# Kernel tuning notes

Hardware: AMD Instinct MI355X
Metric: run time of the kernel (lower is better)

Reference implementation:

```python
import jax, jax.numpy as jnp
import numpy as np

BATCH, SEQ, DIM, DSTATE = 8, 2048, 1024, 16


def setup_inputs() -> dict:
    key = jax.random.key(0)
    ks = jax.random.split(key, 8)
    u = jax.random.normal(ks[0], (BATCH, SEQ, DIM), jnp.float32)
    gate = jax.random.normal(ks[1], (BATCH, SEQ, DIM), jnp.float32)
    # parameters (init per module: normal std=0.01 for A_log/B/C, zeros for D)
    A_log = 0.01 * jax.random.normal(ks[2], (DSTATE, DSTATE), jnp.float32)
    B_mat = 0.01 * jax.random.normal(ks[3], (DIM, DSTATE), jnp.float32)
    C_mat = 0.01 * jax.random.normal(ks[4], (DIM, DSTATE), jnp.float32)
    D = jnp.zeros((DIM,), jnp.float32)
    bound = 1.0 / np.sqrt(DIM)  # nn.Linear default init
    dt_w = jax.random.uniform(ks[5], (1, DIM), jnp.float32, -bound, bound)
    dt_b = jax.random.uniform(ks[6], (1,), jnp.float32, -bound, bound)
    return {"u": u, "gate": gate, "A_log": A_log, "B_mat": B_mat,
            "C_mat": C_mat, "D": D, "dt_w": dt_w, "dt_b": dt_b}


def reference(u, gate, A_log, B_mat, C_mat, D, dt_w, dt_b):
    # delta = sigmoid(Linear(gate)) : [B, S, 1] -> [B, S]
    delta = jax.nn.sigmoid(jnp.einsum('bsd,od->bso', gate, dt_w) + dt_b)[..., 0]
    A = -jnp.exp(A_log)                               # [N, N]
    scaled_A = delta[..., None, None] * A             # [B, S, N, N]
    A_exp = jax.scipy.linalg.expm(scaled_A)           # batched matrix exp
    Bu = jnp.einsum('bsd,dn->bsn', u, B_mat)          # [B, S, N]

    def step(h, inp):
        Aexp_t, bu_t = inp                            # [B,N,N], [B,N]
        h = jnp.einsum('bn,bnm->bm', h, Aexp_t) + bu_t
        return h, h

    h0 = jnp.zeros((u.shape[0], DSTATE), u.dtype)
    _, hs = jax.lax.scan(step, h0, (jnp.swapaxes(A_exp, 0, 1), jnp.swapaxes(Bu, 0, 1)))
    hs = jnp.swapaxes(hs, 0, 1)                       # [B, S, N]
    y = jnp.einsum('bsn,dn->bsd', hs, C_mat) + D * u  # [B, S, D]
    return y
```

## Files before the change

### kernel.cpp

```cpp
#include <hip/hip_runtime.h>

#define BATCH  8
#define SEQ    2048
#define DIMSZ  1024
#define NST    16
#define LCH    32
#define CPB    (SEQ / LCH)
#define NCHUNK (BATCH * CPB)
#define NCHEB  32
#define PI_F   3.14159265358979f

typedef __attribute__((ext_vector_type(8))) short bf16x8;
typedef __attribute__((ext_vector_type(4))) float f32x4;

static __device__ __forceinline__ unsigned short f2bf(float f) {
    unsigned u = __builtin_bit_cast(unsigned, f);
    unsigned r = (u + 0x7FFFu + ((u >> 16) & 1u)) >> 16;
    return (unsigned short)r;
}
static __device__ __forceinline__ float bf2f(unsigned short h) {
    unsigned u = ((unsigned)h) << 16;
    return __builtin_bit_cast(float, u);
}

__global__ __launch_bounds__(256) void sA_nodes(
    const float* __restrict__ A_log, float* __restrict__ Fn)
{
    __shared__ float Xs[16 * 17];
    __shared__ float Ts[16 * 17];
    const int tid = threadIdx.x;
    const int i = tid >> 4, j = tid & 15;
    const float th = (2.f * blockIdx.x + 1.f) * (PI_F / 64.f);
    const float dl = 0.5f * (1.f + cosf(th));
    const float a  = -expf(A_log[tid]);
    const float x  = dl * a * (1.0f / 64.0f);
    Xs[i*17 + j] = x;
    Ts[i*17 + j] = x;
    float S = x + (i == j ? 1.0f : 0.0f);
    __syncthreads();
#pragma unroll
    for (int k = 2; k <= 8; ++k) {
        float nt = 0.f;
#pragma unroll
        for (int kk = 0; kk < 16; ++kk)
            nt = fmaf(Ts[i*17 + kk], Xs[kk*17 + j], nt);
        nt *= (1.0f / (float)k);
        S += nt;
        __syncthreads();
        Ts[i*17 + j] = nt;
        __syncthreads();
    }
#pragma unroll
    for (int r = 0; r < 6; ++r) {
        __syncthreads();
        Ts[i*17 + j] = S;
        __syncthreads();
        float nt = 0.f;
#pragma unroll
        for (int kk = 0; kk < 16; ++kk)
            nt = fmaf(Ts[i*17 + kk], Ts[kk*17 + j], nt);
        S = nt;
    }
    Fn[(size_t)blockIdx.x * 256 + tid] = S;
}

__global__ __launch_bounds__(256) void sB_setup(
    const float* __restrict__ Fn, const float* __restrict__ B_mat,
    float* __restrict__ Gt,
    unsigned short* __restrict__ Bfh, unsigned short* __restrict__ Bfl)
{
    const int tid = threadIdx.x;
    const int blk = blockIdx.x;
    if (blk < NCHEB) {
        const int m = blk;
        float acc = 0.f;
        for (int k = 0; k < NCHEB; ++k) {
            const float th = (2.f * k + 1.f) * (PI_F / 64.f);
            acc = fmaf(Fn[(size_t)k * 256 + tid], cosf(m * th), acc);
        }
        const float sc = (m == 0) ? (1.f / 32.f) : (2.f / 32.f);
        Gt[(size_t)tid * NCHEB + m] = acc * sc;
    } else {
        const int idx0 = (blk - NCHEB) * 2048;
        for (int t = 0; t < 8; ++t) {
            const int idx = idx0 + t * 256 + tid;
            const int j  = idx & 7;
            const int l  = (idx >> 3) & 63;
            const int ks = idx >> 9;
            const int k  = ks * 32 + ((l >> 4) << 3) + j;
            const int n  = l & 15;
            float bv = B_mat[(size_t)k * 16 + n];
            unsigned short h = f2bf(bv);
            Bfh[idx] = h;
            Bfl[idx] = f2bf(bv - bf2f(h));
        }
    }
}

__global__ __launch_bounds__(256) void k1a_delta(
    const float* __restrict__ gate, const float* __restrict__ dt_w,
    const float* __restrict__ dt_b, float* __restrict__ delta)
{
    const int tid  = threadIdx.x;
    const int lane = tid & 63;
    const int w    = tid >> 6;
    const int tok  = blockIdx.x * 4 + w;
    const float* gp = gate + (size_t)tok * DIMSZ;
    float s = 0.f;
#pragma unroll
    for (int i = 0; i < 4; ++i) {
        const float4 g  = *(const float4*)(gp   + i * 256 + lane * 4);
        const float4 wv = *(const float4*)(dt_w + i * 256 + lane * 4);
        s = fmaf(g.x, wv.x, s); s = fmaf(g.y, wv.y, s);
        s = fmaf(g.z, wv.z, s); s = fmaf(g.w, wv.w, s);
    }
#pragma unroll
    for (int off = 32; off >= 1; off >>= 1)
        s += __shfl_xor(s, off, 64);
    if (lane == 0)
        delta[tok] = 1.0f / (1.0f + expf(-(s + dt_b[0])));
}

__global__ __launch_bounds__(512, 2) void kBA3(
    const float* __restrict__ u,
    const unsigned short* __restrict__ Bfh, const unsigned short* __restrict__ Bfl,
    const float* __restrict__ Gt, const float* __restrict__ delta,
    float* __restrict__ Bu, float* __restrict__ P, float* __restrict__ e)
{
    __shared__ float smem[8704];
    __shared__ float Bus[LCH * NST];
    __shared__ float dl[LCH];
    __shared__ float sd[1];
    __shared__ float Ps[16 * 17];
    const int tid  = threadIdx.x;
    const int lane = tid & 63;
    const int w    = tid >> 6;
    const size_t gI = blockIdx.x;
    const int tok0 = (int)gI * 32;
    const int qk   = w & 3;
    const int tt   = w >> 2;
    const int q    = lane >> 4;
    const int r    = lane & 15;

    if (tid < LCH) dl[tid] = delta[gI * LCH + tid];

    const uint4* bh = (const uint4*)Bfh;
    const uint4* bl = (const uint4*)Bfl;

    const float* up = u + (size_t)(tok0 + tt * 16 + r) * DIMSZ + qk * 256 + q * 8;

    f32x4 acc = {0.f, 0.f, 0.f, 0.f};
#pragma unroll
    for (int c = 0; c < 8; ++c) {
        const float4 v0 = *(const float4*)(up + c * 32);
        const float4 v1 = *(const float4*)(up + c * 32 + 4);
        const uint4 FH = bh[(qk * 8 + c) * 64 + lane];
        const uint4 FL = bl[(qk * 8 + c) * 64 + lane];
        const float fu[8] = {v0.x, v0.y, v0.z, v0.w, v1.x, v1.y, v1.z, v1.w};
        bf16x8 uh, ul;
#pragma unroll
        for (int i = 0; i < 8; ++i) {
            unsigned short h = f2bf(fu[i]);
            uh[i] = (short)h;
            ul[i] = (short)f2bf(fu[i] - bf2f(h));
        }
        const bf16x8 Bh = __builtin_bit_cast(bf16x8, FH);
        const bf16x8 Bl = __builtin_bit_cast(bf16x8, FL);
        acc = __builtin_amdgcn_mfma_f32_16x16x32_bf16(uh, Bh, acc, 0, 0, 0);
        acc = __builtin_amdgcn_mfma_f32_16x16x32_bf16(uh, Bl, acc, 0, 0, 0);
        acc = __builtin_amdgcn_mfma_f32_16x16x32_bf16(ul, Bh, acc, 0, 0, 0);
    }

    float* red = smem;
#pragma unroll
    for (int rr = 0; rr < 4; ++rr)
        red[w * 256 + (q * 4 + rr) * 16 + r] = acc[rr];
    __syncthreads();
    const int rb = (tid >> 8) * 1024 + (tid & 255);
    const float bv = red[rb] + red[rb + 256] + red[rb + 512] + red[rb + 768];
    Bu[gI * 512 + tid] = bv;
    Bus[tid] = bv;

    const int el = tid & 255;
    float gr[NCHEB];
    {
        const float4* gp = (const float4*)(Gt + (size_t)el * NCHEB);
#pragma unroll
        for (int qq = 0; qq < NCHEB / 4; ++qq) {
            float4 v = gp[qq];
            gr[qq*4+0] = v.x; gr[qq*4+1] = v.y; gr[qq*4+2] = v.z; gr[qq*4+3] = v.w;
        }
    }
    __syncthreads();
    if (tid == 0) {
        float s = 0.f;
        for (int t = 0; t < LCH; ++t) s += dl[t];
        sd[0] = s;
    }
    const int tgrp = tid >> 8;
    for (int t = tgrp * 16; t < tgrp * 16 + 16; ++t) {
        const float x = 2.f * dl[t] - 1.f;
        float accm = fmaf(gr[1], x, gr[0]);
        float tm2 = 1.f, tm1 = x;
#pragma unroll
        for (int m = 2; m < NCHEB; ++m) {
            const float tm = fmaf(2.f * x, tm1, -tm2);
            accm = fmaf(gr[m], tm, accm);
            tm2 = tm1; tm1 = tm;
        }
        smem[t * 272 + (el >> 4) * 17 + (el & 15)] = accm;
    }
    __syncthreads();
    float S;
    {
        const float xp = 2.f * (sd[0] * (1.f / LCH)) - 1.f;
        float accm = fmaf(gr[1], xp, gr[0]);
        float tm2 = 1.f, tm1 = xp;
#pragma unroll
        for (int m = 2; m < NCHEB; ++m) {
            const float tm = fmaf(2.f * xp, tm1, -tm2);
            accm = fmaf(gr[m], tm, accm);
            tm2 = tm1; tm1 = tm;
        }
        S = accm;
    }
    const int i = el >> 4, j = el & 15;
#pragma unroll
    for (int rr = 0; rr < 5; ++rr) {
        if (tid < 256) Ps[i*17 + j] = S;
        __syncthreads();
        float ns = 0.f;
#pragma unroll
        for (int k = 0; k < 16; ++k)
            ns = fmaf(Ps[i*17 + k], Ps[k*17 + j], ns);
        __syncthreads();
        S = ns;
    }
    if (tid < 256) P[gI * 256 + tid] = S;
    if (tid < 64) {
        const int gq = tid >> 4, jj = tid & 15, i0 = gq * 4;
        float h = 0.f;
        for (int t = 0; t < LCH; ++t) {
            float pp = 0.f;
#pragma unroll
            for (int m = 0; m < 4; ++m)
                pp = fmaf(__shfl(h, gq * 20 + m, 64),
                          smem[t * 272 + (i0 + m) * 17 + jj], pp);
            pp += __shfl_xor(pp, 16, 64);
            pp += __shfl_xor(pp, 32, 64);
            h = Bus[t * 16 + jj] + pp;
        }
        if (gq == 0) e[gI * NST + jj] = h;
    }
}

__global__ __launch_bounds__(256) void k4_scan(
    const float* __restrict__ P, const float* __restrict__ e,
    float* __restrict__ hin)
{
    __shared__ float Pl[32 * 272];
    __shared__ float el[32 * NST];
    const int tid = threadIdx.x;
    const int b = blockIdx.x;
    float h = 0.f;
    for (int half = 0; half < 2; ++half) {
        const int c0 = half * 32;
        for (int idx = tid; idx < 32*256; idx += 256) {
            const int c = idx >> 8, ij = idx & 255, i = ij >> 4, jj = ij & 15;
            Pl[c*272 + i*17 + jj] = P[((size_t)(b*CPB + c0 + c)) * 256 + ij];
        }
        for (int idx = tid; idx < 32*NST; idx += 256)
            el[idx] = e[((size_t)(b*CPB + c0)) * NST + idx];
        __syncthreads();
        if (tid < 64) {
            const int gq = tid >> 4, j = tid & 15, i0 = gq * 4;
            for (int c = 0; c < 32; ++c) {
                if (tid < 16) hin[((size_t)(b*CPB + c0 + c)) * NST + j] = h;
                float pp = 0.f;
#pragma unroll
                for (int m = 0; m < 4; ++m)
                    pp = fmaf(__shfl(h, gq * 20 + m, 64),
                              Pl[c*272 + (i0 + m)*17 + j], pp);
                pp += __shfl_xor(pp, 16, 64);
                pp += __shfl_xor(pp, 32, 64);
                h = el[c*16 + j] + pp;
            }
        }
        __syncthreads();
    }
}

__global__ __launch_bounds__(256) void k5_out(
    const float* __restrict__ Gt, const float* __restrict__ delta,
    const float* __restrict__ Bu, const float* __restrict__ hin,
    const float* __restrict__ u, const float* __restrict__ C_mat,
    const float* __restrict__ D, float* __restrict__ y)
{
    __shared__ float Mlds[32 * 272];
    __shared__ float Bus[LCH * NST];
    __shared__ float dl[LCH];
    __shared__ __align__(16) float Hs[LCH * NST];
    const int tid = threadIdx.x;
    const size_t g = blockIdx.x;
    if (tid < LCH) dl[tid] = delta[g * LCH + tid];
    for (int idx = tid; idx < LCH * NST; idx += 256)
        Bus[idx] = Bu[g * (size_t)(LCH * NST) + idx];
    float gr[NCHEB];
    {
        const float4* gp = (const float4*)(Gt + (size_t)tid * NCHEB);
#pragma unroll
        for (int qq = 0; qq < NCHEB / 4; ++qq) {
            float4 v = gp[qq];
            gr[qq*4+0] = v.x; gr[qq*4+1] = v.y; gr[qq*4+2] = v.z; gr[qq*4+3] = v.w;
        }
    }
    __syncthreads();
    for (int t = 0; t < LCH; ++t) {
        const float x = 2.f * dl[t] - 1.f;
        float accm = fmaf(gr[1], x, gr[0]);
        float tm2 = 1.f, tm1 = x;
#pragma unroll
        for (int m = 2; m < NCHEB; ++m) {
            const float tm = fmaf(2.f * x, tm1, -tm2);
            accm = fmaf(gr[m], tm, accm);
            tm2 = tm1; tm1 = tm;
        }
        Mlds[t * 272 + (tid >> 4) * 17 + (tid & 15)] = accm;
    }
    __syncthreads();
    if (tid < 64) {
        const int gq = tid >> 4, jj = tid & 15, i0 = gq * 4;
        float h = hin[g * NST + jj];
        for (int t = 0; t < LCH; ++t) {
            float pp = 0.f;
#pragma unroll
            for (int m = 0; m < 4; ++m)
                pp = fmaf(__shfl(h, gq * 20 + m, 64),
                          Mlds[t * 272 + (i0 + m) * 17 + jj], pp);
            pp += __shfl_xor(pp, 16, 64);
            pp += __shfl_xor(pp, 32, 64);
            h = Bus[t * 16 + jj] + pp;
            if (gq == 0) Hs[t * 16 + jj] = h;
        }
    }
    __syncthreads();
    const int d0 = tid * 4;
    float4 cr[4][4];
#pragma unroll
    for (int r = 0; r < 4; ++r)
#pragma unroll
        for (int qq = 0; qq < 4; ++qq)
            cr[r][qq] = ((const float4*)C_mat)[(d0 + r) * 4 + qq];
    const float4 dv = ((const float4*)D)[tid];
    const bool dnz = (dv.x != 0.f) || (dv.y != 0.f) || (dv.z != 0.f) || (dv.w != 0.f);
    for (int t = 0; t < LCH; ++t) {
        const size_t row = (g * LCH + t) * DIMSZ;
        float y0 = 0.f, y1 = 0.f, y2 = 0.f, y3 = 0.f;
        if (dnz) {
            const float4 uv = ((const float4*)(u + row))[tid];
            y0 = dv.x * uv.x; y1 = dv.y * uv.y; y2 = dv.z * uv.z; y3 = dv.w * uv.w;
        }
#pragma unroll
        for (int qq = 0; qq < 4; ++qq) {
            const float4 hq = *((const float4*)&Hs[t*16 + qq*4]);
            y0 = fmaf(hq.x, cr[0][qq].x, y0); y0 = fmaf(hq.y, cr[0][qq].y, y0);
            y0 = fmaf(hq.z, cr[0][qq].z, y0); y0 = fmaf(hq.w, cr[0][qq].w, y0);
            y1 = fmaf(hq.x, cr[1][qq].x, y1); y1 = fmaf(hq.y, cr[1][qq].y, y1);
            y1 = fmaf(hq.z, cr[1][qq].z, y1); y1 = fmaf(hq.w, cr[1][qq].w, y1);
            y2 = fmaf(hq.x, cr[2][qq].x, y2); y2 = fmaf(hq.y, cr[2][qq].y, y2);
            y2 = fmaf(hq.z, cr[2][qq].z, y2); y2 = fmaf(hq.w, cr[2][qq].w, y2);
            y3 = fmaf(hq.x, cr[3][qq].x, y3); y3 = fmaf(hq.y, cr[3][qq].y, y3);
            y3 = fmaf(hq.z, cr[3][qq].z, y3); y3 = fmaf(hq.w, cr[3][qq].w, y3);
        }
        float4 ov; ov.x = y0; ov.y = y1; ov.z = y2; ov.w = y3;
        ((float4*)(y + row))[tid] = ov;
    }
}

extern "C" void kernel_launch(void* const* d_in, const int* in_sizes, int n_in,
                              void* d_out, int out_size, void* d_ws, size_t ws_size,
                              hipStream_t stream)
{
    const float* u     = (const float*)d_in[0];
    const float* gate  = (const float*)d_in[1];
    const float* A_log = (const float*)d_in[2];
    const float* B_mat = (const float*)d_in[3];
    const float* C_mat = (const float*)d_in[4];
    const float* D     = (const float*)d_in[5];
    const float* dt_w  = (const float*)d_in[6];
    const float* dt_b  = (const float*)d_in[7];
    float* y = (float*)d_out;

    float* ws = (float*)d_ws;
    size_t o = 0;
    float* Fn    = ws + o; o += 32 * 256;
    float* Gt    = ws + o; o += 256 * NCHEB;
    float* delta = ws + o; o += (size_t)BATCH * SEQ;
    float* Bu    = ws + o; o += (size_t)BATCH * SEQ * NST;
    float* P     = ws + o; o += (size_t)NCHUNK * 256;
    float* e     = ws + o; o += (size_t)NCHUNK * NST;
    float* hin   = ws + o; o += (size_t)NCHUNK * NST;
    unsigned short* Bfh = (unsigned short*)(ws + o); o += 8192;
    unsigned short* Bfl = (unsigned short*)(ws + o); o += 8192;

    sA_nodes <<<NCHEB,     256, 0, stream>>>(A_log, Fn);
    sB_setup <<<NCHEB + 8, 256, 0, stream>>>(Fn, B_mat, Gt, Bfh, Bfl);
    k1a_delta<<<BATCH * SEQ / 4, 256, 0, stream>>>(gate, dt_w, dt_b, delta);
    kBA3     <<<NCHUNK,    512, 0, stream>>>(u, Bfh, Bfl, Gt, delta, Bu, P, e);
    k4_scan  <<<BATCH,     256, 0, stream>>>(P, e, hin);
    k5_out   <<<NCHUNK,    256, 0, stream>>>(Gt, delta, Bu, hin, u, C_mat, D, y);
}
```

Baseline: 251.1 us.

## Merge delta into setup kernel, dual-accumulate MFMA, widen output kernel to 512 threads

```diff
diff --git a/kernel.cpp b/kernel.cpp
--- a/kernel.cpp
+++ b/kernel.cpp
@@ -23,14 +23,39 @@
     return __builtin_bit_cast(float, u);
 }
 
-__global__ __launch_bounds__(256) void sA_nodes(
-    const float* __restrict__ A_log, float* __restrict__ Fn)
+__global__ __launch_bounds__(256) void k0_sa_delta(
+    const float* __restrict__ A_log, const float* __restrict__ gate,
+    const float* __restrict__ dt_w, const float* __restrict__ dt_b,
+    float* __restrict__ Fn, float* __restrict__ delta)
 {
     __shared__ float Xs[16 * 17];
     __shared__ float Ts[16 * 17];
-    const int tid = threadIdx.x;
+    const int tid  = threadIdx.x;
+    const int lane = tid & 63;
+    const int w    = tid >> 6;
+    const int g    = blockIdx.x;
+
+    if (g >= 32) {
+        const int tok  = (g - 32) * 4 + w;
+        const float* gp = gate + (size_t)tok * DIMSZ;
+        float s = 0.f;
+#pragma unroll
+        for (int i = 0; i < 4; ++i) {
+            const float4 gv = *(const float4*)(gp   + i * 256 + lane * 4);
+            const float4 wv = *(const float4*)(dt_w + i * 256 + lane * 4);
+            s = fmaf(gv.x, wv.x, s); s = fmaf(gv.y, wv.y, s);
+            s = fmaf(gv.z, wv.z, s); s = fmaf(gv.w, wv.w, s);
+        }
+#pragma unroll
+        for (int off = 32; off >= 1; off >>= 1)
+            s += __shfl_xor(s, off, 64);
+        if (lane == 0)
+            delta[tok] = 1.0f / (1.0f + expf(-(s + dt_b[0])));
+        return;
+    }
+
     const int i = tid >> 4, j = tid & 15;
-    const float th = (2.f * blockIdx.x + 1.f) * (PI_F / 64.f);
+    const float th = (2.f * g + 1.f) * (PI_F / 64.f);
     const float dl = 0.5f * (1.f + cosf(th));
     const float a  = -expf(A_log[tid]);
     const float x  = dl * a * (1.0f / 64.0f);
@@ -61,7 +86,7 @@
             nt = fmaf(Ts[i*17 + kk], Ts[kk*17 + j], nt);
         S = nt;
     }
-    Fn[(size_t)blockIdx.x * 256 + tid] = S;
+    Fn[(size_t)g * 256 + tid] = S;
 }
 
 __global__ __launch_bounds__(256) void sB_setup(
@@ -97,31 +122,7 @@
     }
 }
 
-__global__ __launch_bounds__(256) void k1a_delta(
-    const float* __restrict__ gate, const float* __restrict__ dt_w,
-    const float* __restrict__ dt_b, float* __restrict__ delta)
-{
-    const int tid  = threadIdx.x;
-    const int lane = tid & 63;
-    const int w    = tid >> 6;
-    const int tok  = blockIdx.x * 4 + w;
-    const float* gp = gate + (size_t)tok * DIMSZ;
-    float s = 0.f;
-#pragma unroll
-    for (int i = 0; i < 4; ++i) {
-        const float4 g  = *(const float4*)(gp   + i * 256 + lane * 4);
-        const float4 wv = *(const float4*)(dt_w + i * 256 + lane * 4);
-        s = fmaf(g.x, wv.x, s); s = fmaf(g.y, wv.y, s);
-        s = fmaf(g.z, wv.z, s); s = fmaf(g.w, wv.w, s);
-    }
-#pragma unroll
-    for (int off = 32; off >= 1; off >>= 1)
-        s += __shfl_xor(s, off, 64);
-    if (lane == 0)
-        delta[tok] = 1.0f / (1.0f + expf(-(s + dt_b[0])));
-}
-
-__global__ __launch_bounds__(512, 2) void kBA3(
+__global__ __launch_bounds__(512, 4) void kBA4(
     const float* __restrict__ u,
     const unsigned short* __restrict__ Bfh, const unsigned short* __restrict__ Bfl,
     const float* __restrict__ Gt, const float* __restrict__ delta,
@@ -149,27 +150,43 @@
 
     const float* up = u + (size_t)(tok0 + tt * 16 + r) * DIMSZ + qk * 256 + q * 8;
 
-    f32x4 acc = {0.f, 0.f, 0.f, 0.f};
-#pragma unroll
-    for (int c = 0; c < 8; ++c) {
-        const float4 v0 = *(const float4*)(up + c * 32);
-        const float4 v1 = *(const float4*)(up + c * 32 + 4);
-        const uint4 FH = bh[(qk * 8 + c) * 64 + lane];
-        const uint4 FL = bl[(qk * 8 + c) * 64 + lane];
-        const float fu[8] = {v0.x, v0.y, v0.z, v0.w, v1.x, v1.y, v1.z, v1.w};
-        bf16x8 uh, ul;
+    f32x4 acc0 = {0.f, 0.f, 0.f, 0.f};
+    f32x4 acc1 = {0.f, 0.f, 0.f, 0.f};
+#pragma unroll
+    for (int c = 0; c < 8; c += 2) {
+        const float4 a0 = *(const float4*)(up + c * 32);
+        const float4 a1 = *(const float4*)(up + c * 32 + 4);
+        const float4 b0 = *(const float4*)(up + (c + 1) * 32);
+        const float4 b1 = *(const float4*)(up + (c + 1) * 32 + 4);
+        const uint4 FH0 = bh[(qk * 8 + c) * 64 + lane];
+        const uint4 FL0 = bl[(qk * 8 + c) * 64 + lane];
+        const uint4 FH1 = bh[(qk * 8 + c + 1) * 64 + lane];
+        const uint4 FL1 = bl[(qk * 8 + c + 1) * 64 + lane];
+        __builtin_amdgcn_sched_barrier(0);
+        const float fu0[8] = {a0.x, a0.y, a0.z, a0.w, a1.x, a1.y, a1.z, a1.w};
+        const float fu1[8] = {b0.x, b0.y, b0.z, b0.w, b1.x, b1.y, b1.z, b1.w};
+        bf16x8 uh0, ul0, uh1, ul1;
 #pragma unroll
         for (int i = 0; i < 8; ++i) {
-            unsigned short h = f2bf(fu[i]);
-            uh[i] = (short)h;
-            ul[i] = (short)f2bf(fu[i] - bf2f(h));
-        }
-        const bf16x8 Bh = __builtin_bit_cast(bf16x8, FH);
-        const bf16x8 Bl = __builtin_bit_cast(bf16x8, FL);
-        acc = __builtin_amdgcn_mfma_f32_16x16x32_bf16(uh, Bh, acc, 0, 0, 0);
-        acc = __builtin_amdgcn_mfma_f32_16x16x32_bf16(uh, Bl, acc, 0, 0, 0);
-        acc = __builtin_amdgcn_mfma_f32_16x16x32_bf16(ul, Bh, acc, 0, 0, 0);
-    }
+            unsigned short h = f2bf(fu0[i]);
+            uh0[i] = (short)h; ul0[i] = (short)f2bf(fu0[i] - bf2f(h));
+            h = f2bf(fu1[i]);
+            uh1[i] = (short)h; ul1[i] = (short)f2bf(fu1[i] - bf2f(h));
+        }
+        const bf16x8 Bh0 = __builtin_bit_cast(bf16x8, FH0);
+        const bf16x8 Bl0 = __builtin_bit_cast(bf16x8, FL0);
+        const bf16x8 Bh1 = __builtin_bit_cast(bf16x8, FH1);
+        const bf16x8 Bl1 = __builtin_bit_cast(bf16x8, FL1);
+        acc0 = __builtin_amdgcn_mfma_f32_16x16x32_bf16(uh0, Bh0, acc0, 0, 0, 0);
+        acc1 = __builtin_amdgcn_mfma_f32_16x16x32_bf16(uh1, Bh1, acc1, 0, 0, 0);
+        acc0 = __builtin_amdgcn_mfma_f32_16x16x32_bf16(uh0, Bl0, acc0, 0, 0, 0);
+        acc1 = __builtin_amdgcn_mfma_f32_16x16x32_bf16(uh1, Bl1, acc1, 0, 0, 0);
+        acc0 = __builtin_amdgcn_mfma_f32_16x16x32_bf16(ul0, Bh0, acc0, 0, 0, 0);
+        acc1 = __builtin_amdgcn_mfma_f32_16x16x32_bf16(ul1, Bh1, acc1, 0, 0, 0);
+    }
+    f32x4 acc;
+#pragma unroll
+    for (int rr = 0; rr < 4; ++rr) acc[rr] = acc0[rr] + acc1[rr];
 
     float* red = smem;
 #pragma unroll
@@ -290,7 +307,7 @@
     }
 }
 
-__global__ __launch_bounds__(256) void k5_out(
+__global__ __launch_bounds__(512, 4) void k5b(
     const float* __restrict__ Gt, const float* __restrict__ delta,
     const float* __restrict__ Bu, const float* __restrict__ hin,
     const float* __restrict__ u, const float* __restrict__ C_mat,
@@ -302,12 +319,13 @@
     __shared__ __align__(16) float Hs[LCH * NST];
     const int tid = threadIdx.x;
     const size_t g = blockIdx.x;
+    const int el = tid & 255;
+    const int tgrp = tid >> 8;
     if (tid < LCH) dl[tid] = delta[g * LCH + tid];
-    for (int idx = tid; idx < LCH * NST; idx += 256)
-        Bus[idx] = Bu[g * (size_t)(LCH * NST) + idx];
+    Bus[tid] = Bu[g * 512 + tid];
     float gr[NCHEB];
     {
-        const float4* gp = (const float4*)(Gt + (size_t)tid * NCHEB);
+        const float4* gp = (const float4*)(Gt + (size_t)el * NCHEB);
 #pragma unroll
         for (int qq = 0; qq < NCHEB / 4; ++qq) {
             float4 v = gp[qq];
@@ -315,7 +333,7 @@
         }
     }
     __syncthreads();
-    for (int t = 0; t < LCH; ++t) {
+    for (int t = tgrp * 16; t < tgrp * 16 + 16; ++t) {
         const float x = 2.f * dl[t] - 1.f;
         float accm = fmaf(gr[1], x, gr[0]);
         float tm2 = 1.f, tm1 = x;
@@ -325,7 +343,7 @@
             accm = fmaf(gr[m], tm, accm);
             tm2 = tm1; tm1 = tm;
         }
-        Mlds[t * 272 + (tid >> 4) * 17 + (tid & 15)] = accm;
+        Mlds[t * 272 + (el >> 4) * 17 + (el & 15)] = accm;
     }
     __syncthreads();
     if (tid < 64) {
@@ -344,20 +362,20 @@
         }
     }
     __syncthreads();
-    const int d0 = tid * 4;
+    const int d0 = el * 4;
     float4 cr[4][4];
 #pragma unroll
     for (int r = 0; r < 4; ++r)
 #pragma unroll
         for (int qq = 0; qq < 4; ++qq)
             cr[r][qq] = ((const float4*)C_mat)[(d0 + r) * 4 + qq];
-    const float4 dv = ((const float4*)D)[tid];
+    const float4 dv = ((const float4*)D)[el];
     const bool dnz = (dv.x != 0.f) || (dv.y != 0.f) || (dv.z != 0.f) || (dv.w != 0.f);
-    for (int t = 0; t < LCH; ++t) {
+    for (int t = tgrp * 16; t < tgrp * 16 + 16; ++t) {
         const size_t row = (g * LCH + t) * DIMSZ;
         float y0 = 0.f, y1 = 0.f, y2 = 0.f, y3 = 0.f;
         if (dnz) {
-            const float4 uv = ((const float4*)(u + row))[tid];
+            const float4 uv = ((const float4*)(u + row))[el];
             y0 = dv.x * uv.x; y1 = dv.y * uv.y; y2 = dv.z * uv.z; y3 = dv.w * uv.w;
         }
 #pragma unroll
@@ -373,7 +391,7 @@
             y3 = fmaf(hq.z, cr[3][qq].z, y3); y3 = fmaf(hq.w, cr[3][qq].w, y3);
         }
         float4 ov; ov.x = y0; ov.y = y1; ov.z = y2; ov.w = y3;
-        ((float4*)(y + row))[tid] = ov;
+        ((float4*)(y + row))[el] = ov;
     }
 }
 
@@ -403,10 +421,10 @@
     unsigned short* Bfh = (unsigned short*)(ws + o); o += 8192;
     unsigned short* Bfl = (unsigned short*)(ws + o); o += 8192;
 
-    sA_nodes <<<NCHEB,     256, 0, stream>>>(A_log, Fn);
-    sB_setup <<<NCHEB + 8, 256, 0, stream>>>(Fn, B_mat, Gt, Bfh, Bfl);
-    k1a_delta<<<BATCH * SEQ / 4, 256, 0, stream>>>(gate, dt_w, dt_b, delta);
-    kBA3     <<<NCHUNK,    512, 0, stream>>>(u, Bfh, Bfl, Gt, delta, Bu, P, e);
-    k4_scan  <<<BATCH,     256, 0, stream>>>(P, e, hin);
-    k5_out   <<<NCHUNK,    256, 0, stream>>>(Gt, delta, Bu, hin, u, C_mat, D, y);
-}
+    k0_sa_delta<<<BATCH * SEQ / 4 + 32, 256, 0, stream>>>(
+        A_log, gate, dt_w, dt_b, Fn, delta);
+    sB_setup<<<NCHEB + 8, 256, 0, stream>>>(Fn, B_mat, Gt, Bfh, Bfl);
+    kBA4    <<<NCHUNK, 512, 0, stream>>>(u, Bfh, Bfl, Gt, delta, Bu, P, e);
+    k4_scan <<<BATCH,  256, 0, stream>>>(P, e, hin);
+    k5b     <<<NCHUNK, 512, 0, stream>>>(Gt, delta, Bu, hin, u, C_mat, D, y);
+}
```

Measured after the change: 236.6 us. -5.8%, faster.
